# Kernel tuning notes

Hardware: AMD Instinct MI355X
Metric: run time of the kernel (lower is better)

The kernel has to match this reference:

```python
import jax, jax.numpy as jnp
import numpy as np

B, H, P, D = 4, 16, 1024, 128

def setup_inputs() -> dict:
    key = jax.random.key(0)
    kq, kk = jax.random.split(key)
    q = jax.random.normal(kq, (B, H, P, D), dtype=jnp.float32)
    k = jax.random.normal(kk, (B, H, P, D), dtype=jnp.float32)
    scale = jnp.full((1,), 1.0 / np.sqrt(D), dtype=jnp.float32)
    return {"q": q, "k": k, "scale": scale}

def reference(q, k, scale):
    # base_fun (SiLU) applied as the basis nonlinearity on q and k,
    # then patch-wise attention scores scaled by `scale`, softmax over keys.
    qb = jax.nn.silu(q)  # [B,H,P,D]
    kb = jax.nn.silu(k)  # [B,H,P,D]
    scores = jnp.einsum('bhpd,bhqd->bhpq', qb, kb) * scale  # [B,H,P,P]
    return jax.nn.softmax(scores, axis=-1)
```

## Files before the change

### kernel.cpp

```cpp
#include <hip/hip_runtime.h>
#include <stdint.h>
#include <stddef.h>

#define BHC 64
#define PP  1024
#define DD  128
#define BM  32
#define BN  128
#define NCH 8
#define LSTR 136

typedef __bf16 bf16x8 __attribute__((ext_vector_type(8)));
typedef float  f32x4  __attribute__((ext_vector_type(4)));

__device__ __forceinline__ unsigned short f2bf(float x) {
    union { float f; uint32_t u; } v; v.f = x;
    uint32_t r = v.u + 0x7FFFu + ((v.u >> 16) & 1u);
    return (unsigned short)(r >> 16);
}

__device__ __forceinline__ float silu_f(float x) {
    return x * __builtin_amdgcn_rcpf(1.f + __expf(-x));
}

__global__ void silu_cast_kernel(const float* __restrict__ q, const float* __restrict__ k,
                                 unsigned short* __restrict__ qb, unsigned short* __restrict__ kb,
                                 int n4each) {
    int stride = gridDim.x * blockDim.x;
    int total  = 2 * n4each;
    for (int i = blockIdx.x * blockDim.x + threadIdx.x; i < total; i += stride) {
        const float4* s; ushort4* d; int j;
        if (i < n4each) { s = (const float4*)q; d = (ushort4*)qb; j = i; }
        else            { s = (const float4*)k; d = (ushort4*)kb; j = i - n4each; }
        float4 x = s[j];
        ushort4 o;
        o.x = f2bf(silu_f(x.x)); o.y = f2bf(silu_f(x.y));
        o.z = f2bf(silu_f(x.z)); o.w = f2bf(silu_f(x.w));
        d[j] = o;
    }
}

__global__ __launch_bounds__(512, 4) void attn_kernel(
        const unsigned short* __restrict__ qb, const unsigned short* __restrict__ kb,
        const float* __restrict__ scale, float* __restrict__ out) {
    __shared__ unsigned short ksm[2][BN * LSTR];
    __shared__ float red_l[BM][4];

    int bx   = blockIdx.x;
    int xcd  = bx & 7;
    int idx  = bx >> 3;
    int bh   = xcd * 8 + (idx >> 5);
    int qblk = idx & 31;

    int t    = threadIdx.x;
    int lane = t & 63;
    int w    = t >> 6;
    int qg2  = w & 1;
    int kq   = w >> 1;
    int l15  = lane & 15;
    int quad = lane >> 4;

    const unsigned short* qg = qb + (size_t)bh * (PP * DD) + (size_t)qblk * (BM * DD);
    const unsigned short* kg = kb + (size_t)bh * (PP * DD);

    bf16x8 qF[4];
#pragma unroll
    for (int kk = 0; kk < 4; ++kk)
        qF[kk] = *(const bf16x8*)(qg + (qg2 * 16 + l15) * DD + kk * 32 + quad * 8);

    f32x4 acc[NCH][2];
#pragma unroll
    for (int c = 0; c < NCH; ++c) {
        acc[c][0] = (f32x4)0.0f;
        acc[c][1] = (f32x4)0.0f;
    }

    int rr = t >> 4, cu = t & 15;
    uint4 f[4];
#pragma unroll
    for (int j = 0; j < 4; ++j)
        f[j] = *(const uint4*)(kg + (size_t)(rr + j * 32) * DD + cu * 8);

#pragma unroll
    for (int c = 0; c < NCH; ++c) {
        int b = c & 1;
#pragma unroll
        for (int j = 0; j < 4; ++j)
            *(uint4*)(&ksm[b][(rr + j * 32) * LSTR + cu * 8]) = f[j];
        __syncthreads();
        if (c < NCH - 1) {
#pragma unroll
            for (int j = 0; j < 4; ++j)
                f[j] = *(const uint4*)(kg + (size_t)((c + 1) * BN + rr + j * 32) * DD + cu * 8);
        }
#pragma unroll
        for (int kt = 0; kt < 2; ++kt) {
            int krow = kq * 32 + kt * 16 + l15;
#pragma unroll
            for (int kk = 0; kk < 4; ++kk) {
                bf16x8 kA = *(const bf16x8*)(&ksm[b][krow * LSTR + kk * 32 + quad * 8]);
                acc[c][kt] = __builtin_amdgcn_mfma_f32_16x16x32_bf16(kA, qF[kk], acc[c][kt], 0, 0, 0);
            }
        }
    }

    float C2 = scale[0] * 1.44269504088896340736f;
    float ssum = 0.f;
#pragma unroll
    for (int c = 0; c < NCH; ++c)
#pragma unroll
        for (int kt = 0; kt < 2; ++kt)
#pragma unroll
            for (int r = 0; r < 4; ++r) {
                float e = exp2f(acc[c][kt][r] * C2);
                acc[c][kt][r] = e;
                ssum += e;
            }
    ssum += __shfl_xor(ssum, 16, 64);
    ssum += __shfl_xor(ssum, 32, 64);
    if (quad == 0) red_l[qg2 * 16 + l15][kq] = ssum;
    __syncthreads();
    float4 p = *(const float4*)(&red_l[qg2 * 16 + l15][0]);
    float inv = 1.0f / ((p.x + p.y) + (p.z + p.w));

    float* og = out + ((size_t)bh << 20) + (size_t)(qblk * BM + qg2 * 16 + l15) * PP;
#pragma unroll
    for (int c = 0; c < NCH; ++c)
#pragma unroll
        for (int kt = 0; kt < 2; ++kt) {
            f32x4 v = acc[c][kt] * inv;
            int key = c * BN + kq * 32 + kt * 16 + quad * 4;
            __builtin_nontemporal_store(v, (f32x4*)(og + key));
        }
}

extern "C" void kernel_launch(void* const* d_in, const int* in_sizes, int n_in,
                              void* d_out, int out_size, void* d_ws, size_t ws_size,
                              hipStream_t stream) {
    const float* q     = (const float*)d_in[0];
    const float* k     = (const float*)d_in[1];
    const float* scale = (const float*)d_in[2];
    float* out = (float*)d_out;

    unsigned short* qb = (unsigned short*)d_ws;
    unsigned short* kb = qb + (size_t)BHC * PP * DD;

    int n4each = (BHC * PP * DD) / 4;
    silu_cast_kernel<<<2048, 256, 0, stream>>>(q, k, qb, kb, n4each);
    attn_kernel<<<2048, 512, 0, stream>>>(qb, kb, scale, out);
}
```

Measured before the change: 362.7 us.

## Use direct global-to-LDS loads, 32x32 MFMA, and per-wave K tiles

Replaces the register-staged, block-shared K tile with per-wave K slices that global_load_lds loads straight into LDS. The slices use an XOR-swizzled layout, and explicit vmcnt waits double-buffer the two halves of the head dimension. The MFMA changes from 16x16x32 to 32x32x16, so each wave computes all 32 query rows against its own 32 keys per chunk, which cuts block-wide barriers and the register round trip. Row sums for the softmax are now reduced with wave shuffles and LDS atomics. Output is written as scalar nontemporal stores, which is less vectorised than the previous f32x4 stores and may raise store cost.

```diff
diff --git a/kernel.cpp b/kernel.cpp
--- a/kernel.cpp
+++ b/kernel.cpp
@@ -6,12 +6,14 @@
 #define PP  1024
 #define DD  128
 #define BM  32
-#define BN  128
-#define NCH 8
-#define LSTR 136
+#define BN  256
+#define NCH 4
 
 typedef __bf16 bf16x8 __attribute__((ext_vector_type(8)));
-typedef float  f32x4  __attribute__((ext_vector_type(4)));
+typedef float  f32x16 __attribute__((ext_vector_type(16)));
+
+#define WAIT_VMCNT(n) asm volatile("s_waitcnt vmcnt(" #n ")" ::: "memory")
+#define WAIT_LGKM0    asm volatile("s_waitcnt lgkmcnt(0)" ::: "memory")
 
 __device__ __forceinline__ unsigned short f2bf(float x) {
     union { float f; uint32_t u; } v; v.f = x;
@@ -43,8 +45,8 @@
 __global__ __launch_bounds__(512, 4) void attn_kernel(
         const unsigned short* __restrict__ qb, const unsigned short* __restrict__ kb,
         const float* __restrict__ scale, float* __restrict__ out) {
-    __shared__ unsigned short ksm[2][BN * LSTR];
-    __shared__ float red_l[BM][4];
+    __shared__ __align__(1024) unsigned short ksm[8][2][32][64];
+    __shared__ float red[BM];
 
     int bx   = blockIdx.x;
     int xcd  = bx & 7;
@@ -55,82 +57,103 @@
     int t    = threadIdx.x;
     int lane = t & 63;
     int w    = t >> 6;
-    int qg2  = w & 1;
-    int kq   = w >> 1;
-    int l15  = lane & 15;
-    int quad = lane >> 4;
+    int l31  = lane & 31;
+    int h    = lane >> 5;
 
-    const unsigned short* qg = qb + (size_t)bh * (PP * DD) + (size_t)qblk * (BM * DD);
-    const unsigned short* kg = kb + (size_t)bh * (PP * DD);
+    const unsigned short* qg  = qb + (size_t)bh * (PP * DD) + (size_t)qblk * (BM * DD);
+    const char*           kgc = (const char*)(kb + (size_t)bh * (PP * DD));
 
-    bf16x8 qF[4];
+#define STAGE(c_, half_)  do {                                                         \
+    _Pragma("unroll")                                                                  \
+    for (int i_ = 0; i_ < 4; ++i_) {                                                   \
+        int key_ = (c_) * BN + w * 32 + i_ * 8 + (lane >> 3);                          \
+        const char* src_ = kgc + (size_t)key_ * 256 + (half_) * 128                    \
+                         + (((lane & 7) * 16) ^ ((lane >> 3) << 4));                   \
+        __builtin_amdgcn_global_load_lds(                                              \
+            (__attribute__((address_space(1))) void*)(src_),                           \
+            (__attribute__((address_space(3))) void*)(&ksm[w][half_][i_ * 8][0]),      \
+            16, 0, 0);                                                                 \
+    }                                                                                  \
+} while (0)
+
+#define LDB(s_) (*(const bf16x8*)((const char*)(&ksm[w][(s_) >> 2][l31][0])            \
+                 + ((((s_) & 3) * 32 + h * 16) ^ ((l31 & 7) << 4))))
+
+    bf16x8 qA[8];
 #pragma unroll
-    for (int kk = 0; kk < 4; ++kk)
-        qF[kk] = *(const bf16x8*)(qg + (qg2 * 16 + l15) * DD + kk * 32 + quad * 8);
+    for (int s = 0; s < 8; ++s)
+        qA[s] = *(const bf16x8*)(qg + l31 * DD + s * 16 + h * 8);
 
-    f32x4 acc[NCH][2];
+    if (t < BM) red[t] = 0.f;
+
+    f32x16 acc[NCH];
 #pragma unroll
-    for (int c = 0; c < NCH; ++c) {
-        acc[c][0] = (f32x4)0.0f;
-        acc[c][1] = (f32x4)0.0f;
-    }
+    for (int c = 0; c < NCH; ++c) acc[c] = (f32x16)0.0f;
 
-    int rr = t >> 4, cu = t & 15;
-    uint4 f[4];
-#pragma unroll
-    for (int j = 0; j < 4; ++j)
-        f[j] = *(const uint4*)(kg + (size_t)(rr + j * 32) * DD + cu * 8);
+    WAIT_VMCNT(0);
+    STAGE(0, 0);
+    STAGE(0, 1);
 
 #pragma unroll
     for (int c = 0; c < NCH; ++c) {
-        int b = c & 1;
-#pragma unroll
-        for (int j = 0; j < 4; ++j)
-            *(uint4*)(&ksm[b][(rr + j * 32) * LSTR + cu * 8]) = f[j];
-        __syncthreads();
-        if (c < NCH - 1) {
-#pragma unroll
-            for (int j = 0; j < 4; ++j)
-                f[j] = *(const uint4*)(kg + (size_t)((c + 1) * BN + rr + j * 32) * DD + cu * 8);
-        }
-#pragma unroll
-        for (int kt = 0; kt < 2; ++kt) {
-            int krow = kq * 32 + kt * 16 + l15;
-#pragma unroll
-            for (int kk = 0; kk < 4; ++kk) {
-                bf16x8 kA = *(const bf16x8*)(&ksm[b][krow * LSTR + kk * 32 + quad * 8]);
-                acc[c][kt] = __builtin_amdgcn_mfma_f32_16x16x32_bf16(kA, qF[kk], acc[c][kt], 0, 0, 0);
-            }
-        }
+        WAIT_VMCNT(4);
+        bf16x8 b0 = LDB(0), b1 = LDB(1), b2 = LDB(2), b3 = LDB(3);
+        WAIT_LGKM0;
+        __builtin_amdgcn_sched_barrier(0);
+        if (c < NCH - 1) STAGE(c + 1, 0);
+        acc[c] = __builtin_amdgcn_mfma_f32_32x32x16_bf16(qA[0], b0, acc[c], 0, 0, 0);
+        acc[c] = __builtin_amdgcn_mfma_f32_32x32x16_bf16(qA[1], b1, acc[c], 0, 0, 0);
+        acc[c] = __builtin_amdgcn_mfma_f32_32x32x16_bf16(qA[2], b2, acc[c], 0, 0, 0);
+        acc[c] = __builtin_amdgcn_mfma_f32_32x32x16_bf16(qA[3], b3, acc[c], 0, 0, 0);
+        if (c < NCH - 1) { WAIT_VMCNT(4); } else { WAIT_VMCNT(0); }
+        bf16x8 b4 = LDB(4), b5 = LDB(5), b6 = LDB(6), b7 = LDB(7);
+        WAIT_LGKM0;
+        __builtin_amdgcn_sched_barrier(0);
+        if (c < NCH - 1) STAGE(c + 1, 1);
+        acc[c] = __builtin_amdgcn_mfma_f32_32x32x16_bf16(qA[4], b4, acc[c], 0, 0, 0);
+        acc[c] = __builtin_amdgcn_mfma_f32_32x32x16_bf16(qA[5], b5, acc[c], 0, 0, 0);
+        acc[c] = __builtin_amdgcn_mfma_f32_32x32x16_bf16(qA[6], b6, acc[c], 0, 0, 0);
+        acc[c] = __builtin_amdgcn_mfma_f32_32x32x16_bf16(qA[7], b7, acc[c], 0, 0, 0);
     }
 
     float C2 = scale[0] * 1.44269504088896340736f;
-    float ssum = 0.f;
+    float p[16];
+#pragma unroll
+    for (int r = 0; r < 16; ++r) p[r] = 0.f;
 #pragma unroll
     for (int c = 0; c < NCH; ++c)
 #pragma unroll
-        for (int kt = 0; kt < 2; ++kt)
+        for (int r = 0; r < 16; ++r) {
+            float e = exp2f(acc[c][r] * C2);
+            acc[c][r] = e;
+            p[r] += e;
+        }
 #pragma unroll
-            for (int r = 0; r < 4; ++r) {
-                float e = exp2f(acc[c][kt][r] * C2);
-                acc[c][kt][r] = e;
-                ssum += e;
-            }
-    ssum += __shfl_xor(ssum, 16, 64);
-    ssum += __shfl_xor(ssum, 32, 64);
-    if (quad == 0) red_l[qg2 * 16 + l15][kq] = ssum;
+    for (int r = 0; r < 16; ++r) {
+        p[r] += __shfl_xor(p[r], 1,  64);
+        p[r] += __shfl_xor(p[r], 2,  64);
+        p[r] += __shfl_xor(p[r], 4,  64);
+        p[r] += __shfl_xor(p[r], 8,  64);
+        p[r] += __shfl_xor(p[r], 16, 64);
+    }
     __syncthreads();
-    float4 p = *(const float4*)(&red_l[qg2 * 16 + l15][0]);
-    float inv = 1.0f / ((p.x + p.y) + (p.z + p.w));
+#pragma unroll
+    for (int r = 0; r < 16; ++r)
+        if (l31 == r) atomicAdd(&red[(r & 3) + 8 * (r >> 2) + 4 * h], p[r]);
+    __syncthreads();
 
-    float* og = out + ((size_t)bh << 20) + (size_t)(qblk * BM + qg2 * 16 + l15) * PP;
+    float invv[16];
+#pragma unroll
+    for (int r = 0; r < 16; ++r)
+        invv[r] = 1.0f / red[(r & 3) + 8 * (r >> 2) + 4 * h];
+
+    float* ob = out + ((size_t)bh << 20) + (size_t)(qblk * BM + 4 * h) * PP + w * 32 + l31;
 #pragma unroll
     for (int c = 0; c < NCH; ++c)
 #pragma unroll
-        for (int kt = 0; kt < 2; ++kt) {
-            f32x4 v = acc[c][kt] * inv;
-            int key = c * BN + kq * 32 + kt * 16 + quad * 4;
-            __builtin_nontemporal_store(v, (f32x4*)(og + key));
+        for (int r = 0; r < 16; ++r) {
+            float v = acc[c][r] * invv[r];
+            __builtin_nontemporal_store(v, ob + (size_t)((r & 3) + 8 * (r >> 2)) * PP + c * BN);
         }
 }
 
```

New measurement: 344.4 us. 1.05x faster.
